# Kernel tuning notes

Measured on AMD Instinct MI355X. Metric: run time of the kernel, lower is better.

Reference implementation:

```python
import jax, jax.numpy as jnp
import numpy as np

H, HKV, D, HID, T = 16, 4, 128, 2048, 4096
THETA = 10000.0
EPS = 1e-5
NEG = -1e30


def setup_inputs() -> dict:
    key = jax.random.key(0)
    ks = jax.random.split(key, 4)
    return {
        "positions": jnp.arange(T, dtype=jnp.int32),
        "hidden_states": jax.random.normal(ks[0], (T, HID), jnp.float32),
        "w_qkv": jax.random.normal(ks[1], ((H + 2 * HKV) * D, HID), jnp.float32) * 0.02,
        "w_o": jax.random.normal(ks[2], (HID, H * D), jnp.float32) * 0.02,
        "q_norm_w": jnp.ones((H * D,), jnp.float32),
        "k_norm_w": jnp.ones((HKV * D,), jnp.float32),
    }


def _rope(pos, x):
    # x: [T, nh, D]; neox-style rotary over full head_dim
    half = D // 2
    inv_freq = 1.0 / (THETA ** (jnp.arange(0, D, 2, dtype=jnp.float32) / D))  # [D/2]
    ang = pos.astype(jnp.float32)[:, None] * inv_freq  # [T, D/2]
    cos = jnp.cos(ang)[:, None, :]
    sin = jnp.sin(ang)[:, None, :]
    x1, x2 = x[..., :half], x[..., half:]
    return jnp.concatenate([x1 * cos - x2 * sin, x2 * cos + x1 * sin], axis=-1)


def _rmsnorm(x, w):
    var = jnp.mean(x * x, axis=-1, keepdims=True)
    return x * jax.lax.rsqrt(var + EPS) * w


def reference(positions, hidden_states, w_qkv, w_o, q_norm_w, k_norm_w):
    qkv = hidden_states @ w_qkv.T  # [T, (H+2*HKV)*D]
    q, k, v = jnp.split(qkv, [H * D, H * D + HKV * D], axis=-1)
    # RoPE per head
    q = _rope(positions, q.reshape(T, H, D)).reshape(T, H * D)
    k = _rope(positions, k.reshape(T, HKV, D)).reshape(T, HKV * D)
    # QK-norm over the flattened (all-heads) q_size / kv_size, as in the module
    q = _rmsnorm(q, q_norm_w)
    k = _rmsnorm(k, k_norm_w)
    qh = q.reshape(T, H, D)
    kh = jnp.repeat(k.reshape(T, HKV, D), H // HKV, axis=1)  # GQA expand
    vh = jnp.repeat(v.reshape(T, HKV, D), H // HKV, axis=1)
    scores = jnp.einsum('qhd,khd->hqk', qh, kh) * (D ** -0.5)  # [H, T, T]
    causal = jnp.tril(jnp.ones((T, T), dtype=bool))
    scores = jnp.where(causal, scores, NEG)
    p = jax.nn.softmax(scores, axis=-1)
    attn = jnp.einsum('hqk,khd->qhd', p, vh).reshape(T, H * D)
    return attn @ w_o.T  # [T, HID]
```

## Files before the change

kernel.cpp:

```cpp
#include <hip/hip_runtime.h>
#include <hip/hip_bf16.h>

#define T_SEQ 4096
#define HID   2048
#define NH    16
#define NKV   4
#define HD    128
#define QKV_N 3072
#define QSCALE 0.12751744f
#define SMAX 24.0f

typedef unsigned short u16;
typedef __bf16 bf16x8 __attribute__((ext_vector_type(8)));
typedef float floatx4 __attribute__((ext_vector_type(4)));
typedef float floatx16 __attribute__((ext_vector_type(16)));

__device__ __forceinline__ float b2f(u16 u) {
  union { unsigned int i; float f; } x; x.i = ((unsigned int)u) << 16; return x.f;
}
__device__ __forceinline__ u16 f2b(float f) {
  union { float f; unsigned int i; } x; x.f = f;
  unsigned int i = x.i;
  unsigned int r = (i + 0x7FFFu + ((i >> 16) & 1u)) >> 16;
  return (u16)r;
}
__device__ __forceinline__ void gload_lds16(const u16* g, u16* lds) {
  __builtin_amdgcn_global_load_lds(
      (const __attribute__((address_space(1))) unsigned int*)g,
      (__attribute__((address_space(3))) unsigned int*)lds, 16, 0, 0);
}

__global__ __launch_bounds__(256) void conv_f32_bf16(const float* __restrict__ src,
                                                     u16* __restrict__ dst, int n8) {
  int i = blockIdx.x * 256 + threadIdx.x;
  if (i >= n8) return;
  const float4* s = (const float4*)(src + (size_t)i * 8);
  float4 a = s[0], b = s[1];
  union { u16 h[8]; uint4 u; } r;
  r.h[0] = f2b(a.x); r.h[1] = f2b(a.y); r.h[2] = f2b(a.z); r.h[3] = f2b(a.w);
  r.h[4] = f2b(b.x); r.h[5] = f2b(b.y); r.h[6] = f2b(b.z); r.h[7] = f2b(b.w);
  *(uint4*)(dst + (size_t)i * 8) = r.u;
}

template <int CF>
__global__ __launch_bounds__(256) void gemm_bt(const u16* __restrict__ A, int lda,
                                               const u16* __restrict__ B, int ldb,
                                               void* __restrict__ Cv, int ldc, int K) {
  __shared__ __align__(16) u16 sA[128 * 32];
  __shared__ __align__(16) u16 sB[128 * 32];
  const int tid = threadIdx.x;
  const int wave = tid >> 6, lane = tid & 63;
  const int row0 = blockIdx.y * 128, col0 = blockIdx.x * 128;
  const int wm = (wave >> 1) * 64, wn = (wave & 1) * 64;
  const int frow = lane & 15, fk = (lane >> 4) * 8;

  floatx4 acc[4][4];
#pragma unroll
  for (int i = 0; i < 4; i++)
#pragma unroll
    for (int j = 0; j < 4; j++) acc[i][j] = (floatx4){0.f, 0.f, 0.f, 0.f};

  const int c0 = wave * 2;
  const int v0 = c0 * 64 + lane;
  const int v1 = v0 + 64;
  const u16* gA0 = A + (size_t)(row0 + (v0 >> 2)) * lda + (v0 & 3) * 8;
  const u16* gA1 = A + (size_t)(row0 + (v1 >> 2)) * lda + (v1 & 3) * 8;
  const u16* gB0 = B + (size_t)(col0 + (v0 >> 2)) * ldb + (v0 & 3) * 8;
  const u16* gB1 = B + (size_t)(col0 + (v1 >> 2)) * ldb + (v1 & 3) * 8;

  for (int k0 = 0; k0 < K; k0 += 32) {
    gload_lds16(gA0 + k0, sA + c0 * 512);
    gload_lds16(gA1 + k0, sA + c0 * 512 + 512);
    gload_lds16(gB0 + k0, sB + c0 * 512);
    gload_lds16(gB1 + k0, sB + c0 * 512 + 512);
    __syncthreads();
    bf16x8 af[4], bfv[4];
#pragma unroll
    for (int i = 0; i < 4; i++) {
      af[i]  = *(const bf16x8*)(sA + (wm + i * 16 + frow) * 32 + fk);
      bfv[i] = *(const bf16x8*)(sB + (wn + i * 16 + frow) * 32 + fk);
    }
#pragma unroll
    for (int i = 0; i < 4; i++)
#pragma unroll
      for (int j = 0; j < 4; j++)
        acc[i][j] = __builtin_amdgcn_mfma_f32_16x16x32_bf16(af[i], bfv[j], acc[i][j], 0, 0, 0);
    __syncthreads();
  }
  const int crow = (lane >> 4) * 4, ccol = lane & 15;
#pragma unroll
  for (int i = 0; i < 4; i++)
#pragma unroll
    for (int j = 0; j < 4; j++)
#pragma unroll
      for (int r = 0; r < 4; r++) {
        int rr = row0 + wm + i * 16 + crow + r;
        int cc = col0 + wn + j * 16 + ccol;
        if (CF) ((float*)Cv)[(size_t)rr * ldc + cc] = acc[i][j][r];
        else    ((u16*)Cv)[(size_t)rr * ldc + cc] = f2b(acc[i][j][r]);
      }
}

__device__ __forceinline__ void fast_sincos(float ang, float* s, float* c) {
  float r = ang * 0.15915494309189535f;
  r -= floorf(r);
  *s = __builtin_amdgcn_sinf(r);
  *c = __builtin_amdgcn_cosf(r);
}

__global__ __launch_bounds__(256) void rope_norm(const int* __restrict__ pos_arr,
                                                 u16* __restrict__ qkv,
                                                 const float* __restrict__ qnw,
                                                 const float* __restrict__ knw) {
  const int t = blockIdx.x;
  const int tid = threadIdx.x;
  const int lane = tid & 63, wave = tid >> 6;
  u16* row = qkv + (size_t)t * QKV_N;
  const float pos = (float)pos_arr[t];

  float qv[8];
  float ssq = 0.f;
#pragma unroll
  for (int i = 0; i < 8; i++) {
    int e = tid * 8 + i;
    int r = e & 127, ih = e & 63;
    float invf = exp2f(-(float)ih * 0.20762050593046015f);
    float ang = pos * invf;
    float s, c;
    fast_sincos(ang, &s, &c);
    float val;
    if (r < 64) val = b2f(row[e]) * c - b2f(row[e + 64]) * s;
    else        val = b2f(row[e]) * c + b2f(row[e - 64]) * s;
    qv[i] = val;
    ssq += val * val;
  }
  float kv[2];
  float ssk = 0.f;
  const u16* krow = row + HID;
#pragma unroll
  for (int i = 0; i < 2; i++) {
    int e = tid * 2 + i;
    int r = e & 127, ih = e & 63;
    float invf = exp2f(-(float)ih * 0.20762050593046015f);
    float ang = pos * invf;
    float s, c;
    fast_sincos(ang, &s, &c);
    float val;
    if (r < 64) val = b2f(krow[e]) * c - b2f(krow[e + 64]) * s;
    else        val = b2f(krow[e]) * c + b2f(krow[e - 64]) * s;
    kv[i] = val;
    ssk += val * val;
  }
#pragma unroll
  for (int off = 1; off < 64; off <<= 1) {
    ssq += __shfl_xor(ssq, off);
    ssk += __shfl_xor(ssk, off);
  }
  __shared__ float rq[4], rk[4];
  if (lane == 0) { rq[wave] = ssq; rk[wave] = ssk; }
  __syncthreads();
  float sq = rq[0] + rq[1] + rq[2] + rq[3];
  float sk = rk[0] + rk[1] + rk[2] + rk[3];
  float qsc = rsqrtf(sq * (1.0f / 2048.0f) + 1e-5f) * QSCALE;
  float ksc = rsqrtf(sk * (1.0f / 512.0f) + 1e-5f);
#pragma unroll
  for (int i = 0; i < 8; i++) {
    int e = tid * 8 + i;
    row[e] = f2b(qv[i] * qsc * qnw[e]);
  }
#pragma unroll
  for (int i = 0; i < 2; i++) {
    int e = tid * 2 + i;
    row[HID + e] = f2b(kv[i] * ksc * knw[e]);
  }
}

__global__ __launch_bounds__(256) void transpose_v(const u16* __restrict__ qkv,
                                                   u16* __restrict__ vt) {
  __shared__ __align__(16) u16 tile[64][136];
  const int tid = threadIdx.x;
  const int h = blockIdx.y;
  const int t0 = blockIdx.x * 64;
#pragma unroll
  for (int p = 0; p < 4; p++) {
    int v = p * 256 + tid;
    int r = v >> 4, c = v & 15;
    const u16* g = qkv + (size_t)(t0 + r) * QKV_N + (HID + NKV * HD) + h * HD + c * 8;
    *(uint4*)(&tile[r][c * 8]) = *(const uint4*)g;
  }
  __syncthreads();
#pragma unroll
  for (int p = 0; p < 4; p++) {
    int v = p * 256 + tid;
    int d = v >> 3, c8 = v & 7;
    union { u16 s[8]; uint4 q; } tmp;
#pragma unroll
    for (int i = 0; i < 8; i++) tmp.s[i] = tile[c8 * 8 + i][d];
    u16* g = vt + ((size_t)h * HD + d) * T_SEQ + t0 + c8 * 8;
    *(uint4*)g = tmp.q;
  }
}

__device__ __forceinline__ void stage_kv(const u16* __restrict__ kbase,
                                         const u16* __restrict__ vbase, int kv0,
                                         u16* sk, u16* sv, int tid) {
  const int w = tid >> 6, lane = tid & 63;
#pragma unroll
  for (int i = 0; i < 4; i++) {
    int c = w * 256 + i * 64 + lane;
    int kv = c >> 4, ch = c & 15;
    const u16* g = kbase + (size_t)(kv0 + kv) * QKV_N + ((ch ^ (kv & 7)) * 8);
    gload_lds16(g, sk + (size_t)(w * 256 + i * 64) * 8);
  }
#pragma unroll
  for (int i = 0; i < 4; i++) {
    int c = w * 256 + i * 64 + lane;
    int d = c >> 3, c2 = c & 7;
    const u16* g = vbase + (size_t)d * T_SEQ + kv0 + ((c2 ^ (d & 7)) * 8);
    gload_lds16(g, sv + (size_t)(w * 256 + i * 64) * 8);
  }
}

__global__ __launch_bounds__(256, 2) void attn_kernel(u16* __restrict__ qkv,
                                                      const u16* __restrict__ vt,
                                                      float* __restrict__ scratch,
                                                      float* __restrict__ lbuf) {
  __shared__ __align__(16) u16 sK[2][64 * 128];
  __shared__ __align__(16) u16 sV[2][128 * 64];
  const int tid = threadIdx.x;
  const int wave = tid >> 6, lane = tid & 63;
  const int bid = blockIdx.x;

  const int x = bid & 7, slot = bid >> 3;
  int h, qt, part = 0;
  bool split;
  if (slot < 80) {
    const int pr = slot / 10, r = slot - pr * 10;
    if (r < 4)      { qt = 31 - 2 * pr; part = r & 1;       h = 2 * x + (r >> 1);       split = true;  }
    else if (r < 6) { qt = 15 - pr;                         h = 2 * x + (r - 4);        split = false; }
    else            { qt = 30 - 2 * pr; part = (r - 6) & 1; h = 2 * x + ((r - 6) >> 1); split = true;  }
  } else {
    const int j = slot - 80;
    qt = 7 - (j >> 1);
    h = 2 * x + (j & 1);
    split = false;
  }
  const int s_begin = (split && part) ? (qt + 1) : 0;
  const int s_end   = split ? (part ? 2 * (qt + 1) : (qt + 1)) : 2 * (qt + 1);

  const int kvh = h >> 2;
  const int ql = lane & 31;
  const int fq2 = lane >> 5;
  const u16* kbase = qkv + HID + (size_t)kvh * HD;
  const u16* vbase = vt + (size_t)kvh * HD * T_SEQ;

  const int qw = qt * 128 + wave * 32;
  const int qmax = qw + 31;
  const int qrow = qw + ql;
  bf16x8 qf[8];
  const u16* qp = qkv + (size_t)qrow * QKV_N + h * HD + fq2 * 8;
#pragma unroll
  for (int kc = 0; kc < 8; kc++) qf[kc] = *(const bf16x8*)(qp + kc * 16);
  floatx16 O[4];
#pragma unroll
  for (int dt = 0; dt < 4; dt++)
#pragma unroll
    for (int r = 0; r < 16; r++) O[dt][r] = 0.f;
  float l_part = 0.f;

  const int nsteps = s_end - s_begin;
  stage_kv(kbase, vbase, s_begin * 64, sK[0], sV[0], tid);
#pragma unroll 1
  for (int st = 0; st < nsteps; st++) {
    const int s = s_begin + st;
    __syncthreads();
    if (st + 1 < nsteps)
      stage_kv(kbase, vbase, (s + 1) * 64, sK[(st + 1) & 1], sV[(st + 1) & 1], tid);
    const int kv0 = s * 64;
    if (kv0 <= qmax) {
      const u16* sk = sK[st & 1];
      const u16* sv = sV[st & 1];
      const int ntv = (kv0 + 32 <= qmax) ? 2 : 1;
#pragma unroll
      for (int nt = 0; nt < 2; nt++) {
        if (nt < ntv) {
          floatx16 S;
#pragma unroll
          for (int r = 0; r < 16; r++) S[r] = -SMAX;
          __builtin_amdgcn_s_setprio(1);
#pragma unroll
          for (int kc = 0; kc < 8; kc++) {
            int ch = (kc * 2 + fq2) ^ (ql & 7);
            bf16x8 kf = *(const bf16x8*)(sk + ((nt * 32 + ql) * 16 + ch) * 8);
            S = __builtin_amdgcn_mfma_f32_32x32x16_bf16(kf, qf[kc], S, 0, 0, 0);
          }
          __builtin_amdgcn_s_setprio(0);
          const bool tmask = (kv0 + nt * 32 + 31) > qw;
#pragma unroll
          for (int r = 0; r < 16; r++) {
            float v = S[r];
            if (tmask) {
              int kvg = kv0 + nt * 32 + (r & 3) + ((r >> 2) << 3) + (fq2 << 2);
              v = (kvg > qrow) ? -1e30f : v;
            }
            float p = __builtin_amdgcn_exp2f(v);
            l_part += p;
            S[r] = p;
          }
          unsigned cp[8];
#pragma unroll
          for (int i = 0; i < 8; i++) {
            unsigned wv;
            asm("v_cvt_pk_bf16_f32 %0, %1, %2"
                : "=v"(wv) : "v"(S[i * 2]), "v"(S[i * 2 + 1]));
            cp[i] = wv;
          }
          union { unsigned u[4]; bf16x8 v; } pf0, pf1;
          {
            auto r0 = __builtin_amdgcn_permlane32_swap(cp[0], cp[2], false, false);
            pf0.u[0] = r0[0]; pf0.u[2] = r0[1];
            auto r1 = __builtin_amdgcn_permlane32_swap(cp[1], cp[3], false, false);
            pf0.u[1] = r1[0]; pf0.u[3] = r1[1];
            auto r2 = __builtin_amdgcn_permlane32_swap(cp[4], cp[6], false, false);
            pf1.u[0] = r2[0]; pf1.u[2] = r2[1];
            auto r3 = __builtin_amdgcn_permlane32_swap(cp[5], cp[7], false, false);
            pf1.u[1] = r3[0]; pf1.u[3] = r3[1];
          }
          __builtin_amdgcn_s_setprio(1);
#pragma unroll
          for (int c = 0; c < 2; c++) {
            bf16x8 pf = c ? pf1.v : pf0.v;
#pragma unroll
            for (int dt = 0; dt < 4; dt++) {
              int ch2 = ((nt * 2 + c) * 2 + fq2) ^ (ql & 7);
              bf16x8 vf = *(const bf16x8*)(sv + ((dt * 32 + ql) * 8 + ch2) * 8);
              O[dt] = __builtin_amdgcn_mfma_f32_32x32x16_bf16(vf, pf, O[dt], 0, 0, 0);
            }
          }
          __builtin_amdgcn_s_setprio(0);
        }
      }
    }
  }
  float l = l_part + __shfl_xor(l_part, 32);
  if (!split) {
    float inv = 1.0f / fmaxf(l, 1e-30f);
    u16* orow = qkv + (size_t)qrow * QKV_N + h * HD;
#pragma unroll
    for (int dt = 0; dt < 4; dt++)
#pragma unroll
      for (int rg = 0; rg < 4; rg++) {
        union { u16 hh[4]; uint2 uu; } wv;
#pragma unroll
        for (int rr = 0; rr < 4; rr++) wv.hh[rr] = f2b(O[dt][rg * 4 + rr] * inv);
        *(uint2*)(orow + dt * 32 + rg * 8 + fq2 * 4) = wv.uu;
      }
  } else {
    const int tile = h * 16 + (qt - 16);
    float* obase = scratch + (size_t)(part * 256 + tile) * 16384 +
                   (size_t)(wave * 32 + ql) * 128;
#pragma unroll
    for (int dt = 0; dt < 4; dt++)
#pragma unroll
      for (int rg = 0; rg < 4; rg++) {
        float4 wv = {O[dt][rg * 4 + 0], O[dt][rg * 4 + 1],
                     O[dt][rg * 4 + 2], O[dt][rg * 4 + 3]};
        *(float4*)(obase + dt * 32 + rg * 8 + fq2 * 4) = wv;
      }
    if (fq2 == 0) lbuf[(part * 256 + tile) * 128 + wave * 32 + ql] = l;
  }
}

__global__ __launch_bounds__(256) void combine_split(const float* __restrict__ scratch,
                                                     const float* __restrict__ lbuf,
                                                     u16* __restrict__ qkv) {
  const int t = blockIdx.x;
  const int h = t >> 4, qt = 16 + (t & 15);
  const int tid = threadIdx.x;
  const int rsub = tid >> 4;
  const int d0 = (tid & 15) * 8;
  const float* s0 = scratch + (size_t)t * 16384;
  const float* s1 = scratch + (size_t)(256 + t) * 16384;
#pragma unroll
  for (int p = 0; p < 8; p++) {
    int r = p * 16 + rsub;
    float l0 = lbuf[t * 128 + r];
    float l1 = lbuf[32768 + t * 128 + r];
    float inv = 1.0f / fmaxf(l0 + l1, 1e-30f);
    const float4* a4 = (const float4*)(s0 + (size_t)r * 128 + d0);
    const float4* b4 = (const float4*)(s1 + (size_t)r * 128 + d0);
    float4 a0 = a4[0], a1 = a4[1];
    float4 b0 = b4[0], b1 = b4[1];
    union { u16 hh[8]; uint4 u; } wv;
    wv.hh[0] = f2b((a0.x + b0.x) * inv); wv.hh[1] = f2b((a0.y + b0.y) * inv);
    wv.hh[2] = f2b((a0.z + b0.z) * inv); wv.hh[3] = f2b((a0.w + b0.w) * inv);
    wv.hh[4] = f2b((a1.x + b1.x) * inv); wv.hh[5] = f2b((a1.y + b1.y) * inv);
    wv.hh[6] = f2b((a1.z + b1.z) * inv); wv.hh[7] = f2b((a1.w + b1.w) * inv);
    *(uint4*)(qkv + (size_t)(qt * 128 + r) * QKV_N + h * HD + d0) = wv.u;
  }
}

extern "C" void kernel_launch(void* const* d_in, const int* in_sizes, int n_in,
                              void* d_out, int out_size, void* d_ws, size_t ws_size,
                              hipStream_t stream) {
  const int* positions = (const int*)d_in[0];
  const float* hidden = (const float*)d_in[1];
  const float* w_qkv = (const float*)d_in[2];
  const float* w_o = (const float*)d_in[3];
  const float* qnw = (const float*)d_in[4];
  const float* knw = (const float*)d_in[5];
  float* out = (float*)d_out;

  u16* qkv  = (u16*)d_ws;
  u16* bufA = qkv + (size_t)T_SEQ * QKV_N;
  u16* bufB = bufA + (size_t)T_SEQ * HID;
  float* lbuf = (float*)(bufB + 2097152);
  float* scratch = out;

  conv_f32_bf16<<<4096, 256, 0, stream>>>(hidden, bufA, T_SEQ * HID / 8);
  conv_f32_bf16<<<3072, 256, 0, stream>>>(w_qkv, bufB, QKV_N * HID / 8);
  gemm_bt<0><<<dim3(QKV_N / 128, T_SEQ / 128), 256, 0, stream>>>(
      bufA, HID, bufB, HID, qkv, QKV_N, HID);
  rope_norm<<<T_SEQ, 256, 0, stream>>>(positions, qkv, qnw, knw);
  conv_f32_bf16<<<2048, 256, 0, stream>>>(w_o, bufA, HID * HID / 8);
  transpose_v<<<dim3(T_SEQ / 64, NKV), 256, 0, stream>>>(qkv, bufB);
  attn_kernel<<<768, 256, 0, stream>>>(qkv, bufB, scratch, lbuf);
  combine_split<<<256, 256, 0, stream>>>(scratch, lbuf, qkv);
  gemm_bt<1><<<dim3(HID / 128, T_SEQ / 128), 256, 0, stream>>>(
      qkv, QKV_N, bufA, HID, out, HID, HID);
}
```

Measured before the change: 379.6 us.

## Read V fragments directly from global memory and raise occupancy to three blocks

The attention kernel no longer stages V tiles into shared memory. Each lane now loads its V^T fragments straight from global memory (through L2/L1) inside the PV MFMA loop. Only K stays double-buffered in LDS, which halves LDS use and lets launch bounds target three blocks per CU. The trade is that V loads now sit on the critical path just before the MFMAs, with global latency and possibly uncoalesced 16-byte reads across rows, instead of being prefetched asynchronously.

```diff
diff --git a/kernel.cpp b/kernel.cpp
--- a/kernel.cpp
+++ b/kernel.cpp
@@ -201,32 +201,11 @@
   }
 }
 
-__device__ __forceinline__ void stage_kv(const u16* __restrict__ kbase,
-                                         const u16* __restrict__ vbase, int kv0,
-                                         u16* sk, u16* sv, int tid) {
-  const int w = tid >> 6, lane = tid & 63;
-#pragma unroll
-  for (int i = 0; i < 4; i++) {
-    int c = w * 256 + i * 64 + lane;
-    int kv = c >> 4, ch = c & 15;
-    const u16* g = kbase + (size_t)(kv0 + kv) * QKV_N + ((ch ^ (kv & 7)) * 8);
-    gload_lds16(g, sk + (size_t)(w * 256 + i * 64) * 8);
-  }
-#pragma unroll
-  for (int i = 0; i < 4; i++) {
-    int c = w * 256 + i * 64 + lane;
-    int d = c >> 3, c2 = c & 7;
-    const u16* g = vbase + (size_t)d * T_SEQ + kv0 + ((c2 ^ (d & 7)) * 8);
-    gload_lds16(g, sv + (size_t)(w * 256 + i * 64) * 8);
-  }
-}
-
-__global__ __launch_bounds__(256, 2) void attn_kernel(u16* __restrict__ qkv,
+__global__ __launch_bounds__(256, 3) void attn_kernel(u16* __restrict__ qkv,
                                                       const u16* __restrict__ vt,
                                                       float* __restrict__ scratch,
                                                       float* __restrict__ lbuf) {
   __shared__ __align__(16) u16 sK[2][64 * 128];
-  __shared__ __align__(16) u16 sV[2][128 * 64];
   const int tid = threadIdx.x;
   const int wave = tid >> 6, lane = tid & 63;
   const int bid = blockIdx.x;
@@ -261,6 +240,10 @@
   const u16* qp = qkv + (size_t)qrow * QKV_N + h * HD + fq2 * 8;
 #pragma unroll
   for (int kc = 0; kc < 8; kc++) qf[kc] = *(const bf16x8*)(qp + kc * 16);
+  const u16* vrow[4];
+#pragma unroll
+  for (int dt = 0; dt < 4; dt++) vrow[dt] = vbase + (size_t)(dt * 32 + ql) * T_SEQ;
+
   floatx16 O[4];
 #pragma unroll
   for (int dt = 0; dt < 4; dt++)
@@ -268,18 +251,34 @@
     for (int r = 0; r < 16; r++) O[dt][r] = 0.f;
   float l_part = 0.f;
 
+  const u16* gk[4];
+#pragma unroll
+  for (int i = 0; i < 4; i++) {
+    int c = wave * 256 + i * 64 + lane;
+    int kv = c >> 4, ch = c & 15;
+    gk[i] = kbase + (size_t)(s_begin * 64 + kv) * QKV_N + ((ch ^ (kv & 7)) * 8);
+  }
+
   const int nsteps = s_end - s_begin;
-  stage_kv(kbase, vbase, s_begin * 64, sK[0], sV[0], tid);
+#pragma unroll
+  for (int i = 0; i < 4; i++) {
+    gload_lds16(gk[i], sK[0] + (wave * 256 + i * 64) * 8);
+    gk[i] += 64 * QKV_N;
+  }
 #pragma unroll 1
   for (int st = 0; st < nsteps; st++) {
     const int s = s_begin + st;
     __syncthreads();
-    if (st + 1 < nsteps)
-      stage_kv(kbase, vbase, (s + 1) * 64, sK[(st + 1) & 1], sV[(st + 1) & 1], tid);
+    if (st + 1 < nsteps) {
+#pragma unroll
+      for (int i = 0; i < 4; i++) {
+        gload_lds16(gk[i], sK[(st + 1) & 1] + (wave * 256 + i * 64) * 8);
+        gk[i] += 64 * QKV_N;
+      }
+    }
     const int kv0 = s * 64;
     if (kv0 <= qmax) {
       const u16* sk = sK[st & 1];
-      const u16* sv = sV[st & 1];
       const int ntv = (kv0 + 32 <= qmax) ? 2 : 1;
 #pragma unroll
       for (int nt = 0; nt < 2; nt++) {
@@ -332,8 +331,8 @@
             bf16x8 pf = c ? pf1.v : pf0.v;
 #pragma unroll
             for (int dt = 0; dt < 4; dt++) {
-              int ch2 = ((nt * 2 + c) * 2 + fq2) ^ (ql & 7);
-              bf16x8 vf = *(const bf16x8*)(sv + ((dt * 32 + ql) * 8 + ch2) * 8);
+              const u16* vp = vrow[dt] + kv0 + ((nt * 2 + c) * 2 + fq2) * 8;
+              bf16x8 vf = *(const bf16x8*)vp;
               O[dt] = __builtin_amdgcn_mfma_f32_32x32x16_bf16(vf, pf, O[dt], 0, 0, 0);
             }
           }
```

New measurement: 482.0 us. 27.0% more time.

## Double-buffer GEMM LDS tiles with BK=64 and XOR swizzle

Applied to the files above, without the earlier changes.

Rewrites the bf16 GEMM main loop to use two LDS buffers, prefetching the next K-tile into the alternate buffer while MFMAs run on the current one, and doubles the K-step from 32 to 64. An XOR swizzle on the LDS layout is meant to avoid bank conflicts on the fragment reads. The aim is to hide global-to-LDS latency and halve the number of barriers. In exchange, LDS use rises to 64KB per block, which may reduce occupancy.

```diff
diff --git a/kernel.cpp b/kernel.cpp
--- a/kernel.cpp
+++ b/kernel.cpp
@@ -46,13 +46,14 @@
 __global__ __launch_bounds__(256) void gemm_bt(const u16* __restrict__ A, int lda,
                                                const u16* __restrict__ B, int ldb,
                                                void* __restrict__ Cv, int ldc, int K) {
-  __shared__ __align__(16) u16 sA[128 * 32];
-  __shared__ __align__(16) u16 sB[128 * 32];
+  __shared__ __align__(16) u16 sA[2][128 * 64];
+  __shared__ __align__(16) u16 sB[2][128 * 64];
   const int tid = threadIdx.x;
   const int wave = tid >> 6, lane = tid & 63;
   const int row0 = blockIdx.y * 128, col0 = blockIdx.x * 128;
   const int wm = (wave >> 1) * 64, wn = (wave & 1) * 64;
-  const int frow = lane & 15, fk = (lane >> 4) * 8;
+  const int frow = lane & 15;
+  const int fkb = (lane >> 4) * 16;
 
   floatx4 acc[4][4];
 #pragma unroll
@@ -60,32 +61,58 @@
 #pragma unroll
     for (int j = 0; j < 4; j++) acc[i][j] = (floatx4){0.f, 0.f, 0.f, 0.f};
 
-  const int c0 = wave * 2;
-  const int v0 = c0 * 64 + lane;
-  const int v1 = v0 + 64;
-  const u16* gA0 = A + (size_t)(row0 + (v0 >> 2)) * lda + (v0 & 3) * 8;
-  const u16* gA1 = A + (size_t)(row0 + (v1 >> 2)) * lda + (v1 & 3) * 8;
-  const u16* gB0 = B + (size_t)(col0 + (v0 >> 2)) * ldb + (v0 & 3) * 8;
-  const u16* gB1 = B + (size_t)(col0 + (v1 >> 2)) * ldb + (v1 & 3) * 8;
-
-  for (int k0 = 0; k0 < K; k0 += 32) {
-    gload_lds16(gA0 + k0, sA + c0 * 512);
-    gload_lds16(gA1 + k0, sA + c0 * 512 + 512);
-    gload_lds16(gB0 + k0, sB + c0 * 512);
-    gload_lds16(gB1 + k0, sB + c0 * 512 + 512);
+  const u16* gA[4];
+  const u16* gB[4];
+  int doff[4];
+#pragma unroll
+  for (int p = 0; p < 4; p++) {
+    int d = (p * 256 + tid) * 16;
+    int row = d >> 7;
+    int c = (d & 127) ^ ((row & 7) << 4);
+    gA[p] = A + (size_t)(row0 + row) * lda + (c >> 1);
+    gB[p] = B + (size_t)(col0 + row) * ldb + (c >> 1);
+    doff[p] = (p * 256 + wave * 64) * 8;
+  }
+
+#pragma unroll
+  for (int p = 0; p < 4; p++) {
+    gload_lds16(gA[p], &sA[0][0] + doff[p]);
+    gload_lds16(gB[p], &sB[0][0] + doff[p]);
+  }
+  __syncthreads();
+  int cur = 0;
+  for (int k0 = 0; k0 < K; k0 += 64) {
+    if (k0 + 64 < K) {
+      u16* san = &sA[cur ^ 1][0];
+      u16* sbn = &sB[cur ^ 1][0];
+#pragma unroll
+      for (int p = 0; p < 4; p++) {
+        gload_lds16(gA[p] + k0 + 64, san + doff[p]);
+        gload_lds16(gB[p] + k0 + 64, sbn + doff[p]);
+      }
+    }
+    const u16* pa = &sA[cur][0];
+    const u16* pb = &sB[cur][0];
+#pragma unroll
+    for (int kk = 0; kk < 2; kk++) {
+      bf16x8 af[4], bfv[4];
+#pragma unroll
+      for (int i = 0; i < 4; i++) {
+        int rowA = wm + i * 16 + frow;
+        int bA = (rowA * 128 + kk * 64 + fkb) ^ ((rowA & 7) << 4);
+        af[i] = *(const bf16x8*)(pa + (bA >> 1));
+        int rowB = wn + i * 16 + frow;
+        int bB = (rowB * 128 + kk * 64 + fkb) ^ ((rowB & 7) << 4);
+        bfv[i] = *(const bf16x8*)(pb + (bB >> 1));
+      }
+#pragma unroll
+      for (int i = 0; i < 4; i++)
+#pragma unroll
+        for (int j = 0; j < 4; j++)
+          acc[i][j] = __builtin_amdgcn_mfma_f32_16x16x32_bf16(af[i], bfv[j], acc[i][j], 0, 0, 0);
+    }
     __syncthreads();
-    bf16x8 af[4], bfv[4];
-#pragma unroll
-    for (int i = 0; i < 4; i++) {
-      af[i]  = *(const bf16x8*)(sA + (wm + i * 16 + frow) * 32 + fk);
-      bfv[i] = *(const bf16x8*)(sB + (wn + i * 16 + frow) * 32 + fk);
-    }
-#pragma unroll
-    for (int i = 0; i < 4; i++)
-#pragma unroll
-      for (int j = 0; j < 4; j++)
-        acc[i][j] = __builtin_amdgcn_mfma_f32_16x16x32_bf16(af[i], bfv[j], acc[i][j], 0, 0, 0);
-    __syncthreads();
+    cur ^= 1;
   }
   const int crow = (lane >> 4) * 4, ccol = lane & 15;
 #pragma unroll
```

Result: faster. 366.5 us (-3.5%).
